# Optimization experiments

Measured on AMD Instinct MI355X. Metric: run time of the kernel, lower is better.

Reference implementation:

```python
import jax, jax.numpy as jnp
import numpy as np

N = 50000   # nodes
E = 800000  # edges
F = 128     # node_features
H = 128     # hid_channel
G = 128     # graphs in batch


def _lin(k, din, dout):
    s = 1.0 / np.sqrt(din)
    return jax.random.uniform(k, (din, dout), jnp.float32, -s, s)


def setup_inputs() -> dict:
    key = jax.random.key(0)
    ks = jax.random.split(key, 16)
    x = jax.random.normal(ks[0], (N, F), jnp.float32)
    edge_list = jax.random.randint(ks[1], (E, 2), 0, N)
    batch = jnp.sort(jax.random.randint(ks[2], (N,), 0, G))
    inp = {"x": x, "edge_list": edge_list, "batch": batch}
    dims = [(F, H)] + [(H, H)] * 4
    for i, (di, do) in enumerate(dims):
        k1, k2 = jax.random.split(ks[3 + i])
        inp[f"Wl{i+1}"] = _lin(k1, di, do)   # weight on aggregated neighbors
        inp[f"Wr{i+1}"] = _lin(k2, di, do)   # root (self) weight
        inp[f"b{i+1}"] = jnp.zeros((do,), jnp.float32)
    inp["Wf1"] = _lin(ks[10], H, H)
    inp["bf1"] = jnp.zeros((H,), jnp.float32)
    inp["Wf2"] = _lin(ks[11], H, 1)
    inp["bf2"] = jnp.zeros((1,), jnp.float32)
    return inp


def reference(x, edge_list, batch,
              Wl1, Wr1, b1, Wl2, Wr2, b2, Wl3, Wr3, b3,
              Wl4, Wr4, b4, Wl5, Wr5, b5, Wf1, bf1, Wf2, bf2):
    src = edge_list[:, 0]  # message source (x_j)
    dst = edge_list[:, 1]  # aggregation target
    ones_e = jnp.ones((E,), x.dtype)
    deg = jnp.clip(jax.ops.segment_sum(ones_e, dst, num_segments=N), 1.0)

    def sage(h, Wl, Wr, b):
        # scatter-mean of neighbor features, then two linears (PyG SAGEConv, aggr='mean')
        agg = jax.ops.segment_sum(h[src], dst, num_segments=N) / deg[:, None]
        return agg @ Wl + h @ Wr + b

    h = x
    for Wl, Wr, b in ((Wl1, Wr1, b1), (Wl2, Wr2, b2), (Wl3, Wr3, b3),
                      (Wl4, Wr4, b4), (Wl5, Wr5, b5)):
        h = jax.nn.relu(sage(h, Wl, Wr, b))

    # global mean pool over graphs
    cnt = jnp.clip(jax.ops.segment_sum(jnp.ones((N,), h.dtype), batch, num_segments=G), 1.0)
    g = jax.ops.segment_sum(h, batch, num_segments=G) / cnt[:, None]

    g = jax.nn.relu(g @ Wf1 + bf1)
    out = jax.nn.sigmoid(g @ Wf2 + bf2)  # num_classes==1 binary path
    return out.reshape(-1)
```

## Files before the change

kernel.cpp:

```cpp
#include <hip/hip_runtime.h>
#include <math.h>

#define N_NODES 50000
#define MPAD    50048
#define N_EDGES 800000
#define FDIM    128
#define NGRAPH  128

#define NCB   196
#define CBN   256
#define ABLK  256
#define EPB   (N_EDGES / ABLK)
#define CVT_BLOCKS ((MPAD * FDIM / 4 + 255) / 256)
#define WCONV_BLOCKS 640

#define NCHUNK 8
#define CHUNK_OF(s) ((int)(((u32)(s) * 671u) >> 22))

typedef __attribute__((ext_vector_type(8))) short short8;
typedef __attribute__((ext_vector_type(4))) float f32x4;
typedef __attribute__((ext_vector_type(2))) float f32x2;
typedef unsigned int u32;

__device__ __forceinline__ unsigned short f2bf(float f) {
    unsigned int u = __float_as_uint(f);
    return (unsigned short)((u + 0x7FFFu + ((u >> 16) & 1u)) >> 16);
}
__device__ __forceinline__ float bfhi(unsigned int u) { return __uint_as_float(u & 0xFFFF0000u); }
__device__ __forceinline__ float bflo(unsigned int u) { return __uint_as_float(u << 16); }

#define ACC16(v) { \
    f32x2 d0 = __builtin_amdgcn_cvt_pk_f32_fp8((int)(v).x, false); \
    f32x2 d1 = __builtin_amdgcn_cvt_pk_f32_fp8((int)(v).x, true);  \
    f32x2 d2 = __builtin_amdgcn_cvt_pk_f32_fp8((int)(v).y, false); \
    f32x2 d3 = __builtin_amdgcn_cvt_pk_f32_fp8((int)(v).y, true);  \
    f32x2 d4 = __builtin_amdgcn_cvt_pk_f32_fp8((int)(v).z, false); \
    f32x2 d5 = __builtin_amdgcn_cvt_pk_f32_fp8((int)(v).z, true);  \
    f32x2 d6 = __builtin_amdgcn_cvt_pk_f32_fp8((int)(v).w, false); \
    f32x2 d7 = __builtin_amdgcn_cvt_pk_f32_fp8((int)(v).w, true);  \
    acc[0] += d0.x;  acc[1] += d0.y;  acc[2] += d1.x;  acc[3] += d1.y; \
    acc[4] += d2.x;  acc[5] += d2.y;  acc[6] += d3.x;  acc[7] += d3.y; \
    acc[8] += d4.x;  acc[9] += d4.y;  acc[10] += d5.x; acc[11] += d5.y; \
    acc[12] += d6.x; acc[13] += d6.y; acc[14] += d7.x; acc[15] += d7.y; }

struct WPtrs { const float* wl[5]; const float* wr[5]; };

__global__ __launch_bounds__(256) void pre_kernel(const float* __restrict__ x,
                                                  unsigned short* __restrict__ xb,
                                                  unsigned char* __restrict__ xb8,
                                                  const int* __restrict__ edges,
                                                  int* __restrict__ g_hist,
                                                  WPtrs wp,
                                                  unsigned short* __restrict__ wcat,
                                                  const int* __restrict__ batch,
                                                  float* __restrict__ gsum,
                                                  float* __restrict__ invcnt) {
    __shared__ int hist[NCB];
    int t = threadIdx.x;
    if (blockIdx.x < CVT_BLOCKS) {
        int i = blockIdx.x * 256 + t;
        if (i >= MPAD * FDIM / 4) return;
        int base = i * 4;
        uint2 o;
        if (base < N_NODES * FDIM) {
            float4 v = *(const float4*)&x[base];
            o.x = (u32)f2bf(v.x) | ((u32)f2bf(v.y) << 16);
            o.y = (u32)f2bf(v.z) | ((u32)f2bf(v.w) << 16);
            int p8 = __builtin_amdgcn_cvt_pk_fp8_f32(v.x, v.y, 0, false);
            p8 = __builtin_amdgcn_cvt_pk_fp8_f32(v.z, v.w, p8, true);
            *(u32*)&xb8[base] = (u32)p8;
        } else { o.x = 0u; o.y = 0u; }
        *(uint2*)&xb[base] = o;
    } else if (blockIdx.x < CVT_BLOCKS + ABLK) {
        int blk = blockIdx.x - CVT_BLOCKS;
        if (t < NCB) hist[t] = 0;
        __syncthreads();
        int beg = blk * EPB, end = beg + EPB;
        for (int i = beg + t; i < end; i += 256) {
            int2 ed = ((const int2*)edges)[i];
            atomicAdd(&hist[ed.y >> 8], 1);
        }
        __syncthreads();
        if (t < NCB) g_hist[t * ABLK + blk] = hist[t];
    } else {
        int tg = (blockIdx.x - CVT_BLOCKS - ABLK) * 256 + t;
        if (tg < NGRAPH * FDIM) gsum[tg] = 0.0f;
        if (tg < NGRAPH) {
            int g = tg;
            int lo = 0, hi = N_NODES;
            while (lo < hi) { int mid = (lo + hi) >> 1; if (batch[mid] < g) lo = mid + 1; else hi = mid; }
            int beg = lo;
            hi = N_NODES;
            while (lo < hi) { int mid = (lo + hi) >> 1; if (batch[mid] < g + 1) lo = mid + 1; else hi = mid; }
            invcnt[g] = 1.0f / (float)max(lo - beg, 1);
        }
        int l = tg >> 15;
        int rem = tg & 32767;
        int k = rem >> 7;
        int n = rem & 127;
        const float* W = (k < 128) ? wp.wl[l] : wp.wr[l];
        float v = W[(k & 127) * 128 + n];
        wcat[((size_t)l << 15) + n * 256 + k] = f2bf(v);
    }
}

__global__ __launch_bounds__(64) void scan1_kernel(const int* __restrict__ g_hist,
                                                   int* __restrict__ g_base,
                                                   int* __restrict__ cbtotal) {
    int cbi = blockIdx.x, l = threadIdx.x;
    int4 v = ((const int4*)(g_hist + cbi * ABLK))[l];
    int s1 = v.x + v.y, s2 = s1 + v.z, s3 = s2 + v.w;
    int inc = s3;
    #pragma unroll
    for (int off = 1; off < 64; off <<= 1) {
        int nv = __shfl_up(inc, off, 64);
        if (l >= off) inc += nv;
    }
    int excl = inc - s3;
    int4 o; o.x = excl; o.y = excl + v.x; o.z = excl + s1; o.w = excl + s2;
    ((int4*)(g_base + cbi * ABLK))[l] = o;
    if (l == 63) cbtotal[cbi] = inc;
}

__global__ __launch_bounds__(256) void scan2_kernel(const int* __restrict__ cbtotal,
                                                    int* __restrict__ cbbase,
                                                    int* __restrict__ row_ptr) {
    __shared__ int s[NCB];
    int t = threadIdx.x;
    if (t < NCB) s[t] = cbtotal[t];
    __syncthreads();
    if (t == 0) {
        int run = 0;
        for (int i = 0; i < NCB; ++i) { int v = s[i]; s[i] = run; run += v; }
        row_ptr[N_NODES] = N_EDGES;
    }
    __syncthreads();
    if (t < NCB) cbbase[t] = s[t];
}

__global__ __launch_bounds__(256) void scatter_kernel(const int* __restrict__ edges,
                                                      const int* __restrict__ g_base,
                                                      const int* __restrict__ cbbase,
                                                      u32* __restrict__ coarse) {
    __shared__ int cur[NCB];
    int t = threadIdx.x, blk = blockIdx.x;
    if (t < NCB) cur[t] = g_base[t * ABLK + blk] + cbbase[t];
    __syncthreads();
    int beg = blk * EPB, end = beg + EPB;
    for (int i = beg + t; i < end; i += 256) {
        int2 ed = ((const int2*)edges)[i];
        int cb = ed.y >> 8;
        int pos = atomicAdd(&cur[cb], 1);
        coarse[pos] = ((u32)(ed.y & 255) << 16) | (u32)ed.x;
    }
}

__global__ __launch_bounds__(256) void csr_kernel(const int* __restrict__ cbbase,
                                                  const int* __restrict__ cbtotal,
                                                  const u32* __restrict__ coarse,
                                                  int* __restrict__ csr_src,
                                                  int* __restrict__ row_ptr,
                                                  float* __restrict__ invdeg) {
    __shared__ int cnt[CBN][NCHUNK];
    __shared__ int dbase[CBN];
    int cb = blockIdx.x, t = threadIdx.x;
    int n = cbtotal[cb], base = cbbase[cb];
    #pragma unroll
    for (int c0 = 0; c0 < NCHUNK; ++c0) cnt[t][c0] = 0;
    __syncthreads();
    const u32* ce = coarse + base;
    for (int i = t; i < n; i += 256) {
        u32 ev = ce[i];
        atomicAdd(&cnt[ev >> 16][CHUNK_OF(ev & 0xFFFFu)], 1);
    }
    __syncthreads();
    {
        int run = 0;
        #pragma unroll
        for (int c0 = 0; c0 < NCHUNK; ++c0) { int v = cnt[t][c0]; cnt[t][c0] = run; run += v; }
        dbase[t] = run;
    }
    __syncthreads();
    if (t == 0) {
        int run = base;
        for (int d = 0; d < CBN; ++d) { int v = dbase[d]; dbase[d] = run; run += v; }
    }
    __syncthreads();
    {
        int db = dbase[t];
        int deg = ((t == CBN - 1) ? base + n : dbase[t + 1]) - db;
        #pragma unroll
        for (int c0 = 0; c0 < NCHUNK; ++c0) cnt[t][c0] += db;
        int node = cb * CBN + t;
        if (node < N_NODES) {
            row_ptr[node] = db;
            invdeg[node] = 1.0f / (float)max(deg, 1);
        }
    }
    __syncthreads();
    for (int i = t; i < n; i += 256) {
        u32 ev = ce[i];
        int pos = atomicAdd(&cnt[ev >> 16][CHUNK_OF(ev & 0xFFFFu)], 1);
        csr_src[pos] = (int)(ev & 0xFFFFu);
    }
}

__global__ __launch_bounds__(256) void sage_fused_kernel(
        const unsigned short* __restrict__ h,
        const unsigned char*  __restrict__ h8,
        const int* __restrict__ row_ptr,
        const int* __restrict__ csr_src,
        const float* __restrict__ invdeg,
        const unsigned short* __restrict__ Wcat,
        const float* __restrict__ bias,
        unsigned short* __restrict__ out,
        unsigned char*  __restrict__ out8,
        const int* __restrict__ pool_batch,
        float* __restrict__ gsum) {
    __shared__ unsigned short As[32][136];
    int t = threadIdx.x;
    int node0 = blockIdx.x * 32;

    {
        int slot = t >> 3;
        int lane = t & 7;
        int c = lane * 16;
        int node = node0 + slot;
        float acc[16];
        #pragma unroll
        for (int i = 0; i < 16; ++i) acc[i] = 0.f;
        if (node < N_NODES) {
            int beg = row_ptr[node], end = row_ptr[node + 1];
            int e = beg;
            for (; e + 4 <= end; e += 4) {
                int s0 = csr_src[e + 0];
                int s1 = csr_src[e + 1];
                int s2 = csr_src[e + 2];
                int s3 = csr_src[e + 3];
                uint4 v0 = *(const uint4*)&h8[(size_t)s0 * FDIM + c];
                uint4 v1 = *(const uint4*)&h8[(size_t)s1 * FDIM + c];
                uint4 v2 = *(const uint4*)&h8[(size_t)s2 * FDIM + c];
                uint4 v3 = *(const uint4*)&h8[(size_t)s3 * FDIM + c];
                ACC16(v0); ACC16(v1); ACC16(v2); ACC16(v3);
            }
            for (; e < end; ++e) {
                int s = csr_src[e];
                uint4 v = *(const uint4*)&h8[(size_t)s * FDIM + c];
                ACC16(v);
            }
            float inv = invdeg[node];
            #pragma unroll
            for (int i = 0; i < 16; ++i) acc[i] *= inv;
        }
        uint4 o0, o1;
        o0.x = (u32)f2bf(acc[0])  | ((u32)f2bf(acc[1])  << 16);
        o0.y = (u32)f2bf(acc[2])  | ((u32)f2bf(acc[3])  << 16);
        o0.z = (u32)f2bf(acc[4])  | ((u32)f2bf(acc[5])  << 16);
        o0.w = (u32)f2bf(acc[6])  | ((u32)f2bf(acc[7])  << 16);
        o1.x = (u32)f2bf(acc[8])  | ((u32)f2bf(acc[9])  << 16);
        o1.y = (u32)f2bf(acc[10]) | ((u32)f2bf(acc[11]) << 16);
        o1.z = (u32)f2bf(acc[12]) | ((u32)f2bf(acc[13]) << 16);
        o1.w = (u32)f2bf(acc[14]) | ((u32)f2bf(acc[15]) << 16);
        *(uint4*)&As[slot][c] = o0;
        *(uint4*)&As[slot][c + 8] = o1;
    }
    __syncthreads();

    int wave = t >> 6;
    int lane = t & 63;
    int l15 = lane & 15;
    int q = lane >> 4;
    int stripe = wave >> 1;
    int half = wave & 1;
    int row_base = node0 + stripe * 16;

    f32x4 acc[4];
    #pragma unroll
    for (int i = 0; i < 4; ++i) acc[i] = (f32x4){0.f, 0.f, 0.f, 0.f};

    {
        const unsigned short* Wb = Wcat + (size_t)(half * 64 + l15) * 256 + q * 8;
        #pragma unroll
        for (int k0 = 0; k0 < 128; k0 += 32) {
            short8 a = *(const short8*)&As[stripe * 16 + l15][q * 8 + k0];
            #pragma unroll
            for (int j = 0; j < 4; ++j) {
                short8 b = *(const short8*)(Wb + (size_t)j * 16 * 256 + k0);
                acc[j] = __builtin_amdgcn_mfma_f32_16x16x32_bf16(a, b, acc[j], 0, 0, 0);
            }
        }
    }
    {
        const unsigned short* Ab = h + (size_t)(row_base + l15) * FDIM + q * 8;
        const unsigned short* Wb = Wcat + (size_t)(half * 64 + l15) * 256 + 128 + q * 8;
        #pragma unroll
        for (int k0 = 0; k0 < 128; k0 += 32) {
            short8 a = *(const short8*)(Ab + k0);
            #pragma unroll
            for (int j = 0; j < 4; ++j) {
                short8 b = *(const short8*)(Wb + (size_t)j * 16 * 256 + k0);
                acc[j] = __builtin_amdgcn_mfma_f32_16x16x32_bf16(a, b, acc[j], 0, 0, 0);
            }
        }
    }

    if (pool_batch == nullptr) {
        #pragma unroll
        for (int j = 0; j < 4; ++j) {
            int col = (half * 4 + j) * 16 + l15;
            float bv = bias[col];
            #pragma unroll
            for (int r = 0; r < 4; ++r) {
                int row = row_base + q * 4 + r;
                float v = fmaxf(acc[j][r] + bv, 0.f);
                out[(size_t)row * FDIM + col] = f2bf(v);
                int pk = __builtin_amdgcn_cvt_pk_fp8_f32(v, v, 0, false);
                out8[(size_t)row * FDIM + col] = (unsigned char)(pk & 0xff);
            }
        }
    } else {
        __syncthreads();
        #pragma unroll
        for (int j = 0; j < 4; ++j) {
            int col = (half * 4 + j) * 16 + l15;
            float bv = bias[col];
            #pragma unroll
            for (int r = 0; r < 4; ++r) {
                int rl = stripe * 16 + q * 4 + r;
                As[rl][col] = f2bf(fmaxf(acc[j][r] + bv, 0.f));
            }
        }
        __syncthreads();
        if (t < FDIM) {
            int f = t;
            int nmax = min(32, N_NODES - node0);
            float a = 0.0f;
            int cur = pool_batch[node0];
            for (int r = 0; r < nmax; ++r) {
                int b = pool_batch[node0 + r];
                if (b != cur) {
                    atomicAdd(&gsum[cur * FDIM + f], a);
                    a = 0.0f;
                    cur = b;
                }
                a += bflo((u32)As[r][f]);
            }
            atomicAdd(&gsum[cur * FDIM + f], a);
        }
    }
}

__global__ void mlp_kernel(const float* __restrict__ gsum,
                           const float* __restrict__ invcnt,
                           const float* __restrict__ Wf1, const float* __restrict__ bf1,
                           const float* __restrict__ Wf2, const float* __restrict__ bf2,
                           float* __restrict__ out) {
    int gg = blockIdx.x;
    int j = threadIdx.x;
    __shared__ float row[128];
    __shared__ float red[128];
    row[j] = gsum[gg * 128 + j] * invcnt[gg];
    __syncthreads();
    float acc = bf1[j];
    for (int k = 0; k < 128; ++k) acc = fmaf(row[k], Wf1[k * 128 + j], acc);
    float v = fmaxf(acc, 0.0f);
    red[j] = v * Wf2[j];
    __syncthreads();
    for (int off = 64; off > 0; off >>= 1) {
        if (j < off) red[j] += red[j + off];
        __syncthreads();
    }
    if (j == 0) out[gg] = 1.0f / (1.0f + expf(-(red[0] + bf2[0])));
}

extern "C" void kernel_launch(void* const* d_in, const int* in_sizes, int n_in,
                              void* d_out, int out_size, void* d_ws, size_t ws_size,
                              hipStream_t stream) {
    const float* x      = (const float*)d_in[0];
    const int*   edges  = (const int*)d_in[1];
    const int*   batch  = (const int*)d_in[2];
    WPtrs wp;
    const float* bs[5];
    for (int l = 0; l < 5; ++l) {
        wp.wl[l] = (const float*)d_in[3 + 3 * l];
        wp.wr[l] = (const float*)d_in[4 + 3 * l];
        bs[l]    = (const float*)d_in[5 + 3 * l];
    }
    const float* Wf1 = (const float*)d_in[18];
    const float* bf1 = (const float*)d_in[19];
    const float* Wf2 = (const float*)d_in[20];
    const float* bf2 = (const float*)d_in[21];
    float* out = (float*)d_out;

    char* ws = (char*)d_ws;
    auto alloc = [&](size_t bytes) { void* p = (void*)ws; ws += (bytes + 255) & ~(size_t)255; return p; };
    unsigned short* xb   = (unsigned short*)alloc((size_t)MPAD * FDIM * 2);
    unsigned short* hA   = (unsigned short*)alloc((size_t)MPAD * FDIM * 2);
    unsigned short* hB   = (unsigned short*)alloc((size_t)MPAD * FDIM * 2);
    unsigned short* wcat = (unsigned short*)alloc((size_t)5 * 128 * 256 * 2);
    u32*   coarse   = (u32*)alloc((size_t)N_EDGES * 4);
    int*   g_hist   = (int*)alloc((size_t)NCB * ABLK * 4);
    int*   g_base   = (int*)alloc((size_t)NCB * ABLK * 4);
    int*   cbbase   = (int*)alloc((size_t)NCB * 4);
    int*   cbtotal  = (int*)alloc((size_t)NCB * 4);
    int*   row_ptr  = (int*)alloc((size_t)(N_NODES + 1) * 4);
    int*   csr_src  = (int*)alloc((size_t)N_EDGES * 4);
    float* invdeg   = (float*)alloc((size_t)N_NODES * 4);
    float* gsum     = (float*)alloc((size_t)NGRAPH * FDIM * 4);
    float* invcnt   = (float*)alloc((size_t)NGRAPH * 4);
    unsigned char* h8A = (unsigned char*)alloc((size_t)MPAD * FDIM);
    unsigned char* xb8 = (unsigned char*)hB;
    unsigned char* h8B = (unsigned char*)xb;
    (void)ws_size; (void)in_sizes; (void)n_in; (void)out_size;

    pre_kernel<<<CVT_BLOCKS + ABLK + WCONV_BLOCKS, 256, 0, stream>>>(
        x, xb, xb8, edges, g_hist, wp, wcat, batch, gsum, invcnt);
    scan1_kernel<<<NCB, 64, 0, stream>>>(g_hist, g_base, cbtotal);
    scan2_kernel<<<1, 256, 0, stream>>>(cbtotal, cbbase, row_ptr);
    scatter_kernel<<<ABLK, 256, 0, stream>>>(edges, g_base, cbbase, coarse);
    csr_kernel<<<NCB, 256, 0, stream>>>(cbbase, cbtotal, coarse, csr_src, row_ptr, invdeg);

    const unsigned short* hcur  = xb;
    const unsigned char*  h8cur = xb8;
    unsigned short* bufs[2]  = {hA, hB};
    unsigned char*  bufs8[2] = {h8A, h8B};
    for (int l = 0; l < 5; ++l) {
        unsigned short* hnext  = bufs[l & 1];
        unsigned char*  h8next = (l == 4) ? nullptr : bufs8[l & 1];
        const int* pb = (l == 4) ? batch : nullptr;
        sage_fused_kernel<<<MPAD / 32, 256, 0, stream>>>(
            hcur, h8cur, row_ptr, csr_src, invdeg, wcat + ((size_t)l << 15), bs[l],
            hnext, h8next, pb, gsum);
        hcur = hnext;
        h8cur = bufs8[l & 1];
    }

    mlp_kernel<<<NGRAPH, 128, 0, stream>>>(gsum, invcnt, Wf1, bf1, Wf2, bf2, out);
}
```

Measured before the change: 387.0 us.

## Split fp8 node features into two 64-column planes for two-pass gather

Stores the fp8 copy of node features as two separate 64-byte-per-node planes (low and high halves of the columns) instead of one 128-byte row. The aggregation loop now makes two passes over each node's neighbor list, gathering 8 bytes per lane from one plane at a time. The intent is to shrink the working set of each pass so the gathered plane fits better in cache. In exchange, the CSR indices are read twice and loop overhead doubles, and each load is now 8 bytes rather than 16.

```diff
diff --git a/kernel.cpp b/kernel.cpp
--- a/kernel.cpp
+++ b/kernel.cpp
@@ -29,25 +29,20 @@
 __device__ __forceinline__ float bfhi(unsigned int u) { return __uint_as_float(u & 0xFFFF0000u); }
 __device__ __forceinline__ float bflo(unsigned int u) { return __uint_as_float(u << 16); }
 
-#define ACC16(v) { \
+#define ACC8(v) { \
     f32x2 d0 = __builtin_amdgcn_cvt_pk_f32_fp8((int)(v).x, false); \
     f32x2 d1 = __builtin_amdgcn_cvt_pk_f32_fp8((int)(v).x, true);  \
     f32x2 d2 = __builtin_amdgcn_cvt_pk_f32_fp8((int)(v).y, false); \
     f32x2 d3 = __builtin_amdgcn_cvt_pk_f32_fp8((int)(v).y, true);  \
-    f32x2 d4 = __builtin_amdgcn_cvt_pk_f32_fp8((int)(v).z, false); \
-    f32x2 d5 = __builtin_amdgcn_cvt_pk_f32_fp8((int)(v).z, true);  \
-    f32x2 d6 = __builtin_amdgcn_cvt_pk_f32_fp8((int)(v).w, false); \
-    f32x2 d7 = __builtin_amdgcn_cvt_pk_f32_fp8((int)(v).w, true);  \
-    acc[0] += d0.x;  acc[1] += d0.y;  acc[2] += d1.x;  acc[3] += d1.y; \
-    acc[4] += d2.x;  acc[5] += d2.y;  acc[6] += d3.x;  acc[7] += d3.y; \
-    acc[8] += d4.x;  acc[9] += d4.y;  acc[10] += d5.x; acc[11] += d5.y; \
-    acc[12] += d6.x; acc[13] += d6.y; acc[14] += d7.x; acc[15] += d7.y; }
+    acc[0] += d0.x; acc[1] += d0.y; acc[2] += d1.x; acc[3] += d1.y; \
+    acc[4] += d2.x; acc[5] += d2.y; acc[6] += d3.x; acc[7] += d3.y; }
 
 struct WPtrs { const float* wl[5]; const float* wr[5]; };
 
 __global__ __launch_bounds__(256) void pre_kernel(const float* __restrict__ x,
                                                   unsigned short* __restrict__ xb,
-                                                  unsigned char* __restrict__ xb8,
+                                                  unsigned char* __restrict__ xb8lo,
+                                                  unsigned char* __restrict__ xb8hi,
                                                   const int* __restrict__ edges,
                                                   int* __restrict__ g_hist,
                                                   WPtrs wp,
@@ -62,15 +57,22 @@
         if (i >= MPAD * FDIM / 4) return;
         int base = i * 4;
         uint2 o;
+        u32 p8v = 0u;
         if (base < N_NODES * FDIM) {
             float4 v = *(const float4*)&x[base];
             o.x = (u32)f2bf(v.x) | ((u32)f2bf(v.y) << 16);
             o.y = (u32)f2bf(v.z) | ((u32)f2bf(v.w) << 16);
             int p8 = __builtin_amdgcn_cvt_pk_fp8_f32(v.x, v.y, 0, false);
             p8 = __builtin_amdgcn_cvt_pk_fp8_f32(v.z, v.w, p8, true);
-            *(u32*)&xb8[base] = (u32)p8;
+            p8v = (u32)p8;
         } else { o.x = 0u; o.y = 0u; }
         *(uint2*)&xb[base] = o;
+        {
+            int node = base >> 7;
+            int col  = base & 127;
+            unsigned char* pl = (col < 64) ? xb8lo : xb8hi;
+            *(u32*)&pl[(size_t)node * 64 + (col & 63)] = p8v;
+        }
     } else if (blockIdx.x < CVT_BLOCKS + ABLK) {
         int blk = blockIdx.x - CVT_BLOCKS;
         if (t < NCB) hist[t] = 0;
@@ -207,14 +209,16 @@
 
 __global__ __launch_bounds__(256) void sage_fused_kernel(
         const unsigned short* __restrict__ h,
-        const unsigned char*  __restrict__ h8,
+        const unsigned char*  __restrict__ h8lo,
+        const unsigned char*  __restrict__ h8hi,
         const int* __restrict__ row_ptr,
         const int* __restrict__ csr_src,
         const float* __restrict__ invdeg,
         const unsigned short* __restrict__ Wcat,
         const float* __restrict__ bias,
         unsigned short* __restrict__ out,
-        unsigned char*  __restrict__ out8,
+        unsigned char*  __restrict__ out8lo,
+        unsigned char*  __restrict__ out8hi,
         const int* __restrict__ pool_batch,
         float* __restrict__ gsum) {
     __shared__ unsigned short As[32][136];
@@ -224,45 +228,45 @@
     {
         int slot = t >> 3;
         int lane = t & 7;
-        int c = lane * 16;
+        int c = lane * 8;
         int node = node0 + slot;
-        float acc[16];
-        #pragma unroll
-        for (int i = 0; i < 16; ++i) acc[i] = 0.f;
+        int beg = 0, end = 0;
+        float inv = 0.f;
         if (node < N_NODES) {
-            int beg = row_ptr[node], end = row_ptr[node + 1];
+            beg = row_ptr[node];
+            end = row_ptr[node + 1];
+            inv = invdeg[node];
+        }
+        #pragma unroll
+        for (int p = 0; p < 2; ++p) {
+            const unsigned char* plane = p ? h8hi : h8lo;
+            float acc[8] = {0.f, 0.f, 0.f, 0.f, 0.f, 0.f, 0.f, 0.f};
             int e = beg;
             for (; e + 4 <= end; e += 4) {
                 int s0 = csr_src[e + 0];
                 int s1 = csr_src[e + 1];
                 int s2 = csr_src[e + 2];
                 int s3 = csr_src[e + 3];
-                uint4 v0 = *(const uint4*)&h8[(size_t)s0 * FDIM + c];
-                uint4 v1 = *(const uint4*)&h8[(size_t)s1 * FDIM + c];
-                uint4 v2 = *(const uint4*)&h8[(size_t)s2 * FDIM + c];
-                uint4 v3 = *(const uint4*)&h8[(size_t)s3 * FDIM + c];
-                ACC16(v0); ACC16(v1); ACC16(v2); ACC16(v3);
+                uint2 v0 = *(const uint2*)&plane[(size_t)s0 * 64 + c];
+                uint2 v1 = *(const uint2*)&plane[(size_t)s1 * 64 + c];
+                uint2 v2 = *(const uint2*)&plane[(size_t)s2 * 64 + c];
+                uint2 v3 = *(const uint2*)&plane[(size_t)s3 * 64 + c];
+                ACC8(v0); ACC8(v1); ACC8(v2); ACC8(v3);
             }
             for (; e < end; ++e) {
                 int s = csr_src[e];
-                uint4 v = *(const uint4*)&h8[(size_t)s * FDIM + c];
-                ACC16(v);
-            }
-            float inv = invdeg[node];
+                uint2 v = *(const uint2*)&plane[(size_t)s * 64 + c];
+                ACC8(v);
+            }
             #pragma unroll
-            for (int i = 0; i < 16; ++i) acc[i] *= inv;
-        }
-        uint4 o0, o1;
-        o0.x = (u32)f2bf(acc[0])  | ((u32)f2bf(acc[1])  << 16);
-        o0.y = (u32)f2bf(acc[2])  | ((u32)f2bf(acc[3])  << 16);
-        o0.z = (u32)f2bf(acc[4])  | ((u32)f2bf(acc[5])  << 16);
-        o0.w = (u32)f2bf(acc[6])  | ((u32)f2bf(acc[7])  << 16);
-        o1.x = (u32)f2bf(acc[8])  | ((u32)f2bf(acc[9])  << 16);
-        o1.y = (u32)f2bf(acc[10]) | ((u32)f2bf(acc[11]) << 16);
-        o1.z = (u32)f2bf(acc[12]) | ((u32)f2bf(acc[13]) << 16);
-        o1.w = (u32)f2bf(acc[14]) | ((u32)f2bf(acc[15]) << 16);
-        *(uint4*)&As[slot][c] = o0;
-        *(uint4*)&As[slot][c + 8] = o1;
+            for (int i = 0; i < 8; ++i) acc[i] *= inv;
+            uint4 o;
+            o.x = (u32)f2bf(acc[0]) | ((u32)f2bf(acc[1]) << 16);
+            o.y = (u32)f2bf(acc[2]) | ((u32)f2bf(acc[3]) << 16);
+            o.z = (u32)f2bf(acc[4]) | ((u32)f2bf(acc[5]) << 16);
+            o.w = (u32)f2bf(acc[6]) | ((u32)f2bf(acc[7]) << 16);
+            *(uint4*)&As[slot][p * 64 + c] = o;
+        }
     }
     __syncthreads();
 
@@ -305,6 +309,7 @@
     }
 
     if (pool_batch == nullptr) {
+        unsigned char* pl = half ? out8hi : out8lo;
         #pragma unroll
         for (int j = 0; j < 4; ++j) {
             int col = (half * 4 + j) * 16 + l15;
@@ -315,7 +320,7 @@
                 float v = fmaxf(acc[j][r] + bv, 0.f);
                 out[(size_t)row * FDIM + col] = f2bf(v);
                 int pk = __builtin_amdgcn_cvt_pk_fp8_f32(v, v, 0, false);
-                out8[(size_t)row * FDIM + col] = (unsigned char)(pk & 0xff);
+                pl[(size_t)row * 64 + (col & 63)] = (unsigned char)(pk & 0xff);
             }
         }
     } else {
@@ -409,30 +414,38 @@
     float* gsum     = (float*)alloc((size_t)NGRAPH * FDIM * 4);
     float* invcnt   = (float*)alloc((size_t)NGRAPH * 4);
     unsigned char* h8A = (unsigned char*)alloc((size_t)MPAD * FDIM);
-    unsigned char* xb8 = (unsigned char*)hB;
-    unsigned char* h8B = (unsigned char*)xb;
+    unsigned char* h8Alo = h8A;
+    unsigned char* h8Ahi = h8A + (size_t)MPAD * 64;
+    unsigned char* xb8lo = (unsigned char*)hB;
+    unsigned char* xb8hi = (unsigned char*)hB + (size_t)MPAD * 64;
+    unsigned char* h8Blo = (unsigned char*)xb;
+    unsigned char* h8Bhi = (unsigned char*)xb + (size_t)MPAD * 64;
     (void)ws_size; (void)in_sizes; (void)n_in; (void)out_size;
 
     pre_kernel<<<CVT_BLOCKS + ABLK + WCONV_BLOCKS, 256, 0, stream>>>(
-        x, xb, xb8, edges, g_hist, wp, wcat, batch, gsum, invcnt);
+        x, xb, xb8lo, xb8hi, edges, g_hist, wp, wcat, batch, gsum, invcnt);
     scan1_kernel<<<NCB, 64, 0, stream>>>(g_hist, g_base, cbtotal);
     scan2_kernel<<<1, 256, 0, stream>>>(cbtotal, cbbase, row_ptr);
     scatter_kernel<<<ABLK, 256, 0, stream>>>(edges, g_base, cbbase, coarse);
     csr_kernel<<<NCB, 256, 0, stream>>>(cbbase, cbtotal, coarse, csr_src, row_ptr, invdeg);
 
-    const unsigned short* hcur  = xb;
-    const unsigned char*  h8cur = xb8;
-    unsigned short* bufs[2]  = {hA, hB};
-    unsigned char*  bufs8[2] = {h8A, h8B};
+    const unsigned short* hcur = xb;
+    const unsigned char*  h8curlo = xb8lo;
+    const unsigned char*  h8curhi = xb8hi;
+    unsigned short* bufs[2] = {hA, hB};
+    unsigned char*  bufs8lo[2] = {h8Alo, h8Blo};
+    unsigned char*  bufs8hi[2] = {h8Ahi, h8Bhi};
     for (int l = 0; l < 5; ++l) {
-        unsigned short* hnext  = bufs[l & 1];
-        unsigned char*  h8next = (l == 4) ? nullptr : bufs8[l & 1];
+        unsigned short* hnext = bufs[l & 1];
+        unsigned char*  h8nlo = (l == 4) ? nullptr : bufs8lo[l & 1];
+        unsigned char*  h8nhi = (l == 4) ? nullptr : bufs8hi[l & 1];
         const int* pb = (l == 4) ? batch : nullptr;
         sage_fused_kernel<<<MPAD / 32, 256, 0, stream>>>(
-            hcur, h8cur, row_ptr, csr_src, invdeg, wcat + ((size_t)l << 15), bs[l],
-            hnext, h8next, pb, gsum);
+            hcur, h8curlo, h8curhi, row_ptr, csr_src, invdeg, wcat + ((size_t)l << 15), bs[l],
+            hnext, h8nlo, h8nhi, pb, gsum);
         hcur = hnext;
-        h8cur = bufs8[l & 1];
+        h8curlo = bufs8lo[l & 1];
+        h8curhi = bufs8hi[l & 1];
     }
 
     mlp_kernel<<<NGRAPH, 128, 0, stream>>>(gsum, invcnt, Wf1, bf1, Wf2, bf2, out);
```

After: 438.1 us. 13.2% more time.

## Quantize gathered neighbor features to FP4 with LDS lookup decode

Applied to the files above, without the earlier changes.

Stores the per-layer copy of node features used for neighbor aggregation as 4-bit E2M1 codes instead of FP8. Decoding goes through a 256-entry shared-memory table that maps each byte to two packed bf16 values. Output stores become nontemporal and use a lane shuffle to pack nibble pairs. This halves the gather traffic in the aggregation phase, at the cost of much coarser quantization of activations, which risks failing the accuracy tolerance, plus extra LDS lookups and ALU work.

```diff
diff --git a/kernel.cpp b/kernel.cpp
--- a/kernel.cpp
+++ b/kernel.cpp
@@ -19,35 +19,41 @@
 
 typedef __attribute__((ext_vector_type(8))) short short8;
 typedef __attribute__((ext_vector_type(4))) float f32x4;
-typedef __attribute__((ext_vector_type(2))) float f32x2;
 typedef unsigned int u32;
 
 __device__ __forceinline__ unsigned short f2bf(float f) {
     unsigned int u = __float_as_uint(f);
     return (unsigned short)((u + 0x7FFFu + ((u >> 16) & 1u)) >> 16);
 }
-__device__ __forceinline__ float bfhi(unsigned int u) { return __uint_as_float(u & 0xFFFF0000u); }
 __device__ __forceinline__ float bflo(unsigned int u) { return __uint_as_float(u << 16); }
 
-#define ACC16(v) { \
-    f32x2 d0 = __builtin_amdgcn_cvt_pk_f32_fp8((int)(v).x, false); \
-    f32x2 d1 = __builtin_amdgcn_cvt_pk_f32_fp8((int)(v).x, true);  \
-    f32x2 d2 = __builtin_amdgcn_cvt_pk_f32_fp8((int)(v).y, false); \
-    f32x2 d3 = __builtin_amdgcn_cvt_pk_f32_fp8((int)(v).y, true);  \
-    f32x2 d4 = __builtin_amdgcn_cvt_pk_f32_fp8((int)(v).z, false); \
-    f32x2 d5 = __builtin_amdgcn_cvt_pk_f32_fp8((int)(v).z, true);  \
-    f32x2 d6 = __builtin_amdgcn_cvt_pk_f32_fp8((int)(v).w, false); \
-    f32x2 d7 = __builtin_amdgcn_cvt_pk_f32_fp8((int)(v).w, true);  \
-    acc[0] += d0.x;  acc[1] += d0.y;  acc[2] += d1.x;  acc[3] += d1.y; \
-    acc[4] += d2.x;  acc[5] += d2.y;  acc[6] += d3.x;  acc[7] += d3.y; \
-    acc[8] += d4.x;  acc[9] += d4.y;  acc[10] += d5.x; acc[11] += d5.y; \
-    acc[12] += d6.x; acc[13] += d6.y; acc[14] += d7.x; acc[15] += d7.y; }
+__device__ __forceinline__ u32 f2fp4(float f) {
+    float a = fabsf(f);
+    u32 c = (u32)(a >= 0.25f) + (u32)(a >= 0.75f) + (u32)(a >= 1.25f) + (u32)(a >= 1.75f)
+          + (u32)(a >= 2.5f)  + (u32)(a >= 3.5f)  + (u32)(a >= 5.0f);
+    return c | (f < 0.f ? 8u : 0u);
+}
+__device__ __forceinline__ u32 fp4top16(u32 nib) {
+    u32 tt = nib & 7u, m = tt & 1u, e = tt >> 1;
+    u32 h = e ? (((126u + e) << 7) | (m << 6)) : (m * 0x3F00u);
+    return h | ((nib & 8u) << 12);
+}
+
+#define DEC8(ww, off) { \
+    u32 l0 = lut[(ww) & 0xFFu]; \
+    u32 l1 = lut[((ww) >> 8) & 0xFFu]; \
+    u32 l2 = lut[((ww) >> 16) & 0xFFu]; \
+    u32 l3 = lut[(ww) >> 24]; \
+    acc[(off)+0] += __uint_as_float(l0 << 16); acc[(off)+1] += __uint_as_float(l0 & 0xFFFF0000u); \
+    acc[(off)+2] += __uint_as_float(l1 << 16); acc[(off)+3] += __uint_as_float(l1 & 0xFFFF0000u); \
+    acc[(off)+4] += __uint_as_float(l2 << 16); acc[(off)+5] += __uint_as_float(l2 & 0xFFFF0000u); \
+    acc[(off)+6] += __uint_as_float(l3 << 16); acc[(off)+7] += __uint_as_float(l3 & 0xFFFF0000u); }
 
 struct WPtrs { const float* wl[5]; const float* wr[5]; };
 
 __global__ __launch_bounds__(256) void pre_kernel(const float* __restrict__ x,
                                                   unsigned short* __restrict__ xb,
-                                                  unsigned char* __restrict__ xb8,
+                                                  unsigned char* __restrict__ xb4,
                                                   const int* __restrict__ edges,
                                                   int* __restrict__ g_hist,
                                                   WPtrs wp,
@@ -62,15 +68,16 @@
         if (i >= MPAD * FDIM / 4) return;
         int base = i * 4;
         uint2 o;
+        unsigned short p4 = 0;
         if (base < N_NODES * FDIM) {
             float4 v = *(const float4*)&x[base];
             o.x = (u32)f2bf(v.x) | ((u32)f2bf(v.y) << 16);
             o.y = (u32)f2bf(v.z) | ((u32)f2bf(v.w) << 16);
-            int p8 = __builtin_amdgcn_cvt_pk_fp8_f32(v.x, v.y, 0, false);
-            p8 = __builtin_amdgcn_cvt_pk_fp8_f32(v.z, v.w, p8, true);
-            *(u32*)&xb8[base] = (u32)p8;
+            p4 = (unsigned short)(f2fp4(v.x) | (f2fp4(v.y) << 4) |
+                                  (f2fp4(v.z) << 8) | (f2fp4(v.w) << 12));
         } else { o.x = 0u; o.y = 0u; }
         *(uint2*)&xb[base] = o;
+        *(unsigned short*)&xb4[base >> 1] = p4;
     } else if (blockIdx.x < CVT_BLOCKS + ABLK) {
         int blk = blockIdx.x - CVT_BLOCKS;
         if (t < NCB) hist[t] = 0;
@@ -207,19 +214,26 @@
 
 __global__ __launch_bounds__(256) void sage_fused_kernel(
         const unsigned short* __restrict__ h,
-        const unsigned char*  __restrict__ h8,
+        const unsigned char*  __restrict__ h4,
         const int* __restrict__ row_ptr,
         const int* __restrict__ csr_src,
         const float* __restrict__ invdeg,
         const unsigned short* __restrict__ Wcat,
         const float* __restrict__ bias,
         unsigned short* __restrict__ out,
-        unsigned char*  __restrict__ out8,
+        unsigned char*  __restrict__ out4,
         const int* __restrict__ pool_batch,
         float* __restrict__ gsum) {
     __shared__ unsigned short As[32][136];
+    __shared__ u32 lut[256];
     int t = threadIdx.x;
     int node0 = blockIdx.x * 32;
+
+    {
+        u32 b = (u32)t;
+        lut[t] = fp4top16(b & 0xFu) | (fp4top16(b >> 4) << 16);
+    }
+    __syncthreads();
 
     {
         int slot = t >> 3;
@@ -237,16 +251,19 @@
                 int s1 = csr_src[e + 1];
                 int s2 = csr_src[e + 2];
                 int s3 = csr_src[e + 3];
-                uint4 v0 = *(const uint4*)&h8[(size_t)s0 * FDIM + c];
-                uint4 v1 = *(const uint4*)&h8[(size_t)s1 * FDIM + c];
-                uint4 v2 = *(const uint4*)&h8[(size_t)s2 * FDIM + c];
-                uint4 v3 = *(const uint4*)&h8[(size_t)s3 * FDIM + c];
-                ACC16(v0); ACC16(v1); ACC16(v2); ACC16(v3);
+                uint2 w0 = *(const uint2*)&h4[(size_t)s0 * 64 + lane * 8];
+                uint2 w1 = *(const uint2*)&h4[(size_t)s1 * 64 + lane * 8];
+                uint2 w2 = *(const uint2*)&h4[(size_t)s2 * 64 + lane * 8];
+                uint2 w3 = *(const uint2*)&h4[(size_t)s3 * 64 + lane * 8];
+                DEC8(w0.x, 0); DEC8(w0.y, 8);
+                DEC8(w1.x, 0); DEC8(w1.y, 8);
+                DEC8(w2.x, 0); DEC8(w2.y, 8);
+                DEC8(w3.x, 0); DEC8(w3.y, 8);
             }
             for (; e < end; ++e) {
                 int s = csr_src[e];
-                uint4 v = *(const uint4*)&h8[(size_t)s * FDIM + c];
-                ACC16(v);
+                uint2 w = *(const uint2*)&h4[(size_t)s * 64 + lane * 8];
+                DEC8(w.x, 0); DEC8(w.y, 8);
             }
             float inv = invdeg[node];
             #pragma unroll
@@ -295,7 +312,7 @@
         const unsigned short* Wb = Wcat + (size_t)(half * 64 + l15) * 256 + 128 + q * 8;
         #pragma unroll
         for (int k0 = 0; k0 < 128; k0 += 32) {
-            short8 a = *(const short8*)(Ab + k0);
+            short8 a = __builtin_nontemporal_load((const short8*)(Ab + k0));
             #pragma unroll
             for (int j = 0; j < 4; ++j) {
                 short8 b = *(const short8*)(Wb + (size_t)j * 16 * 256 + k0);
@@ -313,9 +330,12 @@
             for (int r = 0; r < 4; ++r) {
                 int row = row_base + q * 4 + r;
                 float v = fmaxf(acc[j][r] + bv, 0.f);
-                out[(size_t)row * FDIM + col] = f2bf(v);
-                int pk = __builtin_amdgcn_cvt_pk_fp8_f32(v, v, 0, false);
-                out8[(size_t)row * FDIM + col] = (unsigned char)(pk & 0xff);
+                __builtin_nontemporal_store(f2bf(v), &out[(size_t)row * FDIM + col]);
+                u32 code = f2fp4(v);
+                u32 pc = (u32)__shfl_xor((int)code, 1);
+                if ((l15 & 1) == 0)
+                    __builtin_nontemporal_store((unsigned char)(code | (pc << 4)),
+                                                &out4[(size_t)row * 64 + (col >> 1)]);
             }
         }
     } else {
@@ -408,31 +428,31 @@
     float* invdeg   = (float*)alloc((size_t)N_NODES * 4);
     float* gsum     = (float*)alloc((size_t)NGRAPH * FDIM * 4);
     float* invcnt   = (float*)alloc((size_t)NGRAPH * 4);
-    unsigned char* h8A = (unsigned char*)alloc((size_t)MPAD * FDIM);
-    unsigned char* xb8 = (unsigned char*)hB;
-    unsigned char* h8B = (unsigned char*)xb;
+    unsigned char* h4A = (unsigned char*)alloc((size_t)MPAD * 64);
+    unsigned char* xb4 = (unsigned char*)hB;
+    unsigned char* h4B = (unsigned char*)xb;
     (void)ws_size; (void)in_sizes; (void)n_in; (void)out_size;
 
     pre_kernel<<<CVT_BLOCKS + ABLK + WCONV_BLOCKS, 256, 0, stream>>>(
-        x, xb, xb8, edges, g_hist, wp, wcat, batch, gsum, invcnt);
+        x, xb, xb4, edges, g_hist, wp, wcat, batch, gsum, invcnt);
     scan1_kernel<<<NCB, 64, 0, stream>>>(g_hist, g_base, cbtotal);
     scan2_kernel<<<1, 256, 0, stream>>>(cbtotal, cbbase, row_ptr);
     scatter_kernel<<<ABLK, 256, 0, stream>>>(edges, g_base, cbbase, coarse);
     csr_kernel<<<NCB, 256, 0, stream>>>(cbbase, cbtotal, coarse, csr_src, row_ptr, invdeg);
 
     const unsigned short* hcur  = xb;
-    const unsigned char*  h8cur = xb8;
+    const unsigned char*  h4cur = xb4;
     unsigned short* bufs[2]  = {hA, hB};
-    unsigned char*  bufs8[2] = {h8A, h8B};
+    unsigned char*  bufs4[2] = {h4A, h4B};
     for (int l = 0; l < 5; ++l) {
         unsigned short* hnext  = bufs[l & 1];
-        unsigned char*  h8next = (l == 4) ? nullptr : bufs8[l & 1];
+        unsigned char*  h4next = (l == 4) ? nullptr : bufs4[l & 1];
         const int* pb = (l == 4) ? batch : nullptr;
         sage_fused_kernel<<<MPAD / 32, 256, 0, stream>>>(
-            hcur, h8cur, row_ptr, csr_src, invdeg, wcat + ((size_t)l << 15), bs[l],
-            hnext, h8next, pb, gsum);
+            hcur, h4cur, row_ptr, csr_src, invdeg, wcat + ((size_t)l << 15), bs[l],
+            hnext, h4next, pb, gsum);
         hcur = hnext;
-        h8cur = bufs8[l & 1];
+        h4cur = bufs4[l & 1];
     }
 
     mlp_kernel<<<NGRAPH, 128, 0, stream>>>(gsum, invcnt, Wf1, bf1, Wf2, bf2, out);
```

Result: slower. 422.8 us (+9.2%).
